# Performance work log

Hardware: AMD Instinct MI355X
Metric: run time of the kernel (lower is better)

Reference implementation:

```python
import jax, jax.numpy as jnp
import numpy as np

K = 1024      # num_embeddings
D = 256       # embedding_dim
BETA = 0.25
DECAY = 0.99
EPS = 1e-05


def setup_inputs() -> dict:
    key = jax.random.key(0)
    k1, k2 = jax.random.split(key)
    z_e = jax.random.normal(k1, (32, D, 32, 32), dtype=jnp.float32)
    embedding = jax.random.normal(k2, (K, D), dtype=jnp.float32)
    ema_cluster_size = jnp.zeros((K,), dtype=jnp.float32)
    ema_w = embedding  # buffer initialized as a clone of the codebook
    return {"z_e": z_e, "embedding": embedding,
            "ema_cluster_size": ema_cluster_size, "ema_w": ema_w}


def reference(z_e, embedding, ema_cluster_size, ema_w):
    B, Dd, H, W = z_e.shape
    # (B, D, H, W) -> (N, D)
    flat_z = jnp.transpose(z_e, (0, 2, 3, 1)).reshape(-1, Dd)

    # L2 distance argmin (||z||^2 + ||e||^2 - 2 z.e)
    dist = (jnp.sum(flat_z * flat_z, axis=1, keepdims=True)
            + jnp.sum(embedding * embedding, axis=1)
            - 2.0 * flat_z @ embedding.T)
    indices = jnp.argmin(dist, axis=1)  # (N,)

    # EMA update (operates on detached values; buffers updated in-place in torch)
    flat_z_sg = jax.lax.stop_gradient(flat_z)
    cluster_size = jax.ops.segment_sum(
        jnp.ones_like(indices, dtype=z_e.dtype), indices, num_segments=K)
    new_ema_cluster_size = DECAY * ema_cluster_size + (1.0 - DECAY) * cluster_size
    dw = jax.ops.segment_sum(flat_z_sg, indices, num_segments=K)  # one_hot.T @ flat_z
    new_ema_w = DECAY * ema_w + (1.0 - DECAY) * dw
    new_embedding = new_ema_w / (new_ema_cluster_size + EPS)[:, None]

    # Gather uses the *updated* codebook (torch copies into the buffer first)
    z_q_flat = new_embedding[indices]                      # (N, D)
    z_q = jnp.transpose(z_q_flat.reshape(B, H, W, Dd), (0, 3, 1, 2))

    # Straight-through estimator + commitment loss
    z_q_st = z_e + jax.lax.stop_gradient(z_q - z_e)
    vq_loss = BETA * jnp.mean((z_e - jax.lax.stop_gradient(z_q)) ** 2)

    return (z_q_st, vq_loss, indices.reshape(B, H, W),
            new_embedding, new_ema_cluster_size, new_ema_w)
```

## Files before the change

### kernel.cpp

```cpp
#include <hip/hip_runtime.h>
#include <stdint.h>

#define N_ROWS 32768
#define K_CODES 1024
#define D_DIM 256
#define NELEM 8388608

#define WS_COUNTS 0
#define WS_LOSS 1030
#define WS_ENORM 263168
#define WS_ROWBEST_BYTES 1056768
#define WS_IDX_BYTES 1318912

#define O_ZQ 0
#define O_LOSS 8388608
#define O_IDX 8388609
#define O_EMB 8421377
#define O_CS 8683521
#define O_EMAW 8684545

#define EP_BYTE_OFF 33685520

typedef _Float16 half8 __attribute__((ext_vector_type(8)));
typedef float f32x16 __attribute__((ext_vector_type(16)));

__device__ __forceinline__ unsigned int fenc(float f) {
    unsigned int u = __float_as_uint(f);
    return (u & 0x80000000u) ? ~u : (u | 0x80000000u);
}
__device__ __forceinline__ unsigned long long umin64(unsigned long long a, unsigned long long b) {
    return a < b ? a : b;
}
__device__ __forceinline__ void gll16(const void* g, void* l) {
    __builtin_amdgcn_global_load_lds((const __attribute__((address_space(1))) void*)g,
                                     (__attribute__((address_space(3))) void*)l, 16, 0, 0);
}

__global__ __launch_bounds__(256) void k_init(float* ws) {
    int i = blockIdx.x * 256 + threadIdx.x;
    if (i < 2048) ws[i] = 0.0f;
    unsigned long long* rb = (unsigned long long*)((char*)ws + WS_ROWBEST_BYTES);
    if (i < N_ROWS) rb[i] = 0xFFFFFFFFFFFFFFFFull;
}

__global__ __launch_bounds__(256) void k_conv_e(const float* __restrict__ emb,
                                                _Float16* __restrict__ Ep,
                                                float* __restrict__ enorm) {
    int k = blockIdx.x, d = threadIdx.x;
    float v = emb[k * 256 + d];
    _Float16 h = (_Float16)v;
    _Float16 l = (_Float16)(v - (float)h);
    int s = d >> 3, sub = d & 7;
    Ep[((size_t)s * 1024 + k) * 8 + sub] = h;
    Ep[((size_t)(32 + s) * 1024 + k) * 8 + sub] = l;
    float sq = v * v;
    #pragma unroll
    for (int off = 32; off >= 1; off >>= 1) sq += __shfl_down(sq, off, 64);
    __shared__ float red[4];
    if ((d & 63) == 0) red[d >> 6] = sq;
    __syncthreads();
    if (d == 0) enorm[k] = (red[0] + red[1]) + (red[2] + red[3]);
}

__global__ __launch_bounds__(256) void k_conv_z(const float* __restrict__ z_e,
                                                _Float16* __restrict__ Zp,
                                                float* __restrict__ lossacc) {
    __shared__ float lt[64 * 68];
    __shared__ float red[4];
    int t = threadIdx.x;
    int hw0 = blockIdx.x * 64, d0 = blockIdx.y * 64, b = blockIdx.z;
    const float* src = z_e + (size_t)b * 262144 + (size_t)d0 * 1024 + hw0;
    int dl = t >> 4, hl = (t & 15) * 4;
    float sq = 0.0f;
    #pragma unroll
    for (int i = 0; i < 4; i++) {
        int d = dl + i * 16;
        float4 v = *(const float4*)(src + (size_t)d * 1024 + hl);
        sq += v.x * v.x + v.y * v.y + v.z * v.z + v.w * v.w;
        lt[(hl + 0) * 68 + d] = v.x;
        lt[(hl + 1) * 68 + d] = v.y;
        lt[(hl + 2) * 68 + d] = v.z;
        lt[(hl + 3) * 68 + d] = v.w;
    }
    __syncthreads();
    int hr = t >> 2, seg = t & 3;
    int n = b * 1024 + hw0 + hr;
    int sg0 = (d0 >> 3) + seg * 2;
    half8 hi[2], lo[2];
    #pragma unroll
    for (int p = 0; p < 2; p++) {
        #pragma unroll
        for (int j = 0; j < 8; j++) {
            float v = lt[hr * 68 + seg * 16 + p * 8 + j];
            _Float16 h = (_Float16)v;
            hi[p][j] = h;
            lo[p][j] = (_Float16)(v - (float)h);
        }
    }
    *(half8*)(Zp + ((size_t)(sg0 + 0) * 32768 + n) * 8) = hi[0];
    *(half8*)(Zp + ((size_t)(sg0 + 1) * 32768 + n) * 8) = hi[1];
    *(half8*)(Zp + ((size_t)(32 + sg0) * 32768 + n) * 8) = lo[0];
    *(half8*)(Zp + ((size_t)(33 + sg0) * 32768 + n) * 8) = lo[1];
    #pragma unroll
    for (int off = 32; off >= 1; off >>= 1) sq += __shfl_down(sq, off, 64);
    if ((t & 63) == 0) red[t >> 6] = sq;
    __syncthreads();
    if (t == 0) atomicAdd(lossacc, (red[0] + red[1]) + (red[2] + red[3]));
}

__global__ __launch_bounds__(256) void k_mm(const _Float16* __restrict__ Zp,
                                            const _Float16* __restrict__ Ep,
                                            const float* __restrict__ enorm,
                                            unsigned long long* __restrict__ row_best) {
    __shared__ __align__(16) char smem[32768];
    _Float16* Za = (_Float16*)smem;
    _Float16* Ea = (_Float16*)(smem + 16384);
    unsigned long long* slot = (unsigned long long*)smem;

    int t = threadIdx.x;
    int lane = t & 63, wv = t >> 6;
    int b = blockIdx.x;
    int rt = (b & 7) + ((b >> 6) << 3);
    int ct = (b >> 3) & 7;
    int row0 = rt * 128, code0 = ct * 128;

    int wr = wv >> 1, wc = wv & 1;
    int m31 = lane & 31, ko = lane >> 5;

    f32x16 acc[2][2];
    #pragma unroll
    for (int i = 0; i < 2; i++)
        #pragma unroll
        for (int j = 0; j < 2; j++)
            #pragma unroll
            for (int r = 0; r < 16; r++) acc[i][j][r] = 0.0f;

    const char* zgl = (const char*)Zp + ((size_t)(2 * wv) * 32768 + row0 + lane) * 16;
    const char* egl = (const char*)Ep + ((size_t)(2 * wv) * 1024 + code0 + lane) * 16;
    _Float16* zld = Za + 2 * wv * 1024;
    _Float16* eld = Ea + 2 * wv * 1024;

    for (int c = 0; c < 12; c++) {
        int kz = (c < 8) ? c : (c - 8);
        int ge = (c < 4) ? c * 8 : (c < 8) ? (c - 4) * 8 : 32 + (c - 8) * 8;
        const char* zg = zgl + (size_t)kz * 8 * 32768 * 16;
        const char* eg = egl + (size_t)ge * 1024 * 16;
        gll16(zg, zld);
        gll16(zg + 64 * 16, zld + 512);
        gll16(zg + 32768 * 16, zld + 1024);
        gll16(zg + 32768 * 16 + 64 * 16, zld + 1536);
        gll16(eg, eld);
        gll16(eg + 64 * 16, eld + 512);
        gll16(eg + 1024 * 16, eld + 1024);
        gll16(eg + 1024 * 16 + 64 * 16, eld + 1536);
        __syncthreads();
        #pragma unroll
        for (int ks = 0; ks < 4; ks++) {
            int sseg = 2 * ks + ko;
            half8 a0 = *(const half8*)(Za + sseg * 1024 + (wr * 64 + m31) * 8);
            half8 a1 = *(const half8*)(Za + sseg * 1024 + (wr * 64 + 32 + m31) * 8);
            half8 b0 = *(const half8*)(Ea + sseg * 1024 + (wc * 64 + m31) * 8);
            half8 b1 = *(const half8*)(Ea + sseg * 1024 + (wc * 64 + 32 + m31) * 8);
            acc[0][0] = __builtin_amdgcn_mfma_f32_32x32x16_f16(a0, b0, acc[0][0], 0, 0, 0);
            acc[0][1] = __builtin_amdgcn_mfma_f32_32x32x16_f16(a0, b1, acc[0][1], 0, 0, 0);
            acc[1][0] = __builtin_amdgcn_mfma_f32_32x32x16_f16(a1, b0, acc[1][0], 0, 0, 0);
            acc[1][1] = __builtin_amdgcn_mfma_f32_32x32x16_f16(a1, b1, acc[1][1], 0, 0, 0);
        }
        __syncthreads();
    }

    float en0 = enorm[code0 + wc * 64 + m31];
    float en1 = enorm[code0 + wc * 64 + 32 + m31];
    unsigned int col0 = code0 + wc * 64 + m31;
    unsigned int col1 = col0 + 32;

    if (wc == 0) {
        #pragma unroll
        for (int mt = 0; mt < 2; mt++)
            #pragma unroll
            for (int j = 0; j < 16; j++) {
                int row = wr * 64 + mt * 32 + 4 * ko + (j & 3) + 8 * (j >> 2);
                unsigned long long p0 = ((unsigned long long)fenc(en0 - 2.0f * acc[mt][0][j]) << 32) | col0;
                unsigned long long p1 = ((unsigned long long)fenc(en1 - 2.0f * acc[mt][1][j]) << 32) | col1;
                slot[row * 32 + ((m31 + row) & 31)] = umin64(p0, p1);
            }
    }
    __syncthreads();
    if (wc == 1) {
        #pragma unroll
        for (int mt = 0; mt < 2; mt++)
            #pragma unroll
            for (int j = 0; j < 16; j++) {
                int row = wr * 64 + mt * 32 + 4 * ko + (j & 3) + 8 * (j >> 2);
                unsigned long long p0 = ((unsigned long long)fenc(en0 - 2.0f * acc[mt][0][j]) << 32) | col0;
                unsigned long long p1 = ((unsigned long long)fenc(en1 - 2.0f * acc[mt][1][j]) << 32) | col1;
                atomicMin(&slot[row * 32 + ((m31 + row) & 31)], umin64(p0, p1));
            }
    }
    __syncthreads();
    if (t < 128) {
        unsigned long long m = slot[t * 32 + (t & 31)];
        #pragma unroll
        for (int i = 1; i < 32; i++) m = umin64(m, slot[t * 32 + ((i + t) & 31)]);
        atomicMin(&row_best[row0 + t], m);
    }
}

__global__ __launch_bounds__(256) void k_fin_idx(const unsigned long long* __restrict__ rb,
                                                 int* __restrict__ idxs,
                                                 float* __restrict__ counts,
                                                 float* __restrict__ out) {
    __shared__ float hist[K_CODES];
    int t = threadIdx.x;
    #pragma unroll
    for (int j = 0; j < 4; j++) hist[j * 256 + t] = 0.0f;
    __syncthreads();
    int i = blockIdx.x * 256 + t;
    int id = (int)(rb[i] & 0xFFFFFFFFull);
    idxs[i] = id;
    out[O_IDX + i] = (float)id;
    atomicAdd(&hist[id], 1.0f);
    __syncthreads();
    #pragma unroll
    for (int j = 0; j < 4; j++) {
        float h = hist[j * 256 + t];
        if (h != 0.0f) atomicAdd(&counts[j * 256 + t], h);
    }
}

__global__ __launch_bounds__(256) void k_dw(const float* __restrict__ z_e,
                                            const int* __restrict__ idxs,
                                            float* __restrict__ part) {
    __shared__ float acc[K_CODES];
    int t = threadIdx.x;
    int s = blockIdx.x;
    int d = blockIdx.y;
    #pragma unroll
    for (int j = 0; j < 4; j++) acc[j * 256 + t] = 0.0f;
    __syncthreads();
    #pragma unroll
    for (int i = 0; i < 4; i++) {
        int b = s * 4 + i;
        int4 id4 = *(const int4*)(idxs + b * 1024 + t * 4);
        float4 v = *(const float4*)(z_e + (size_t)b * 262144 + (size_t)d * 1024 + t * 4);
        atomicAdd(&acc[id4.x], v.x);
        atomicAdd(&acc[id4.y], v.y);
        atomicAdd(&acc[id4.z], v.z);
        atomicAdd(&acc[id4.w], v.w);
    }
    __syncthreads();
    float* pr = part + ((size_t)s * 256 + d) * 1024;
    #pragma unroll
    for (int j = 0; j < 4; j++) pr[j * 256 + t] = acc[j * 256 + t];
}

__global__ __launch_bounds__(256) void k_red(const float* __restrict__ part,
                                             const float* __restrict__ ema_cs,
                                             const float* __restrict__ ema_w,
                                             const float* __restrict__ counts,
                                             float* __restrict__ lossacc,
                                             float* __restrict__ out) {
    __shared__ float tile[64 * 69];
    __shared__ float csl[64];
    __shared__ float craw[64];
    __shared__ float red[4];
    int t = threadIdx.x;
    int k0 = blockIdx.x * 64, d0 = blockIdx.y * 64;
    int dr = t >> 4, kc = t & 15;
    float4 sum[4] = {};
    for (int s = 0; s < 8; s++) {
        const float* pb = part + ((size_t)s * 256 + d0) * 1024 + k0 + kc * 4;
        #pragma unroll
        for (int q = 0; q < 4; q++) {
            float4 v = *(const float4*)(pb + (size_t)(dr + 16 * q) * 1024);
            sum[q].x += v.x; sum[q].y += v.y; sum[q].z += v.z; sum[q].w += v.w;
        }
    }
    if (t < 64) {
        float c = counts[k0 + t];
        craw[t] = c;
        csl[t] = 0.99f * ema_cs[k0 + t] + 0.01f * c;
    }
    #pragma unroll
    for (int q = 0; q < 4; q++) {
        float* p = tile + (dr + 16 * q) * 69 + kc * 4;
        p[0] = sum[q].x; p[1] = sum[q].y; p[2] = sum[q].z; p[3] = sum[q].w;
    }
    __syncthreads();
    int kk = t >> 2, dq = t & 3;
    int k = k0 + kk;
    float inv = 1.0f / (csl[kk] + 1e-5f);
    float cr = craw[kk];
    float lterm = 0.0f;
    #pragma unroll
    for (int j4 = 0; j4 < 4; j4++) {
        int dd = dq * 16 + j4 * 4;
        size_t kd = (size_t)k * 256 + d0 + dd;
        float4 w = *(const float4*)(ema_w + kd);
        float s0 = tile[(dd + 0) * 69 + kk];
        float s1 = tile[(dd + 1) * 69 + kk];
        float s2 = tile[(dd + 2) * 69 + kk];
        float s3 = tile[(dd + 3) * 69 + kk];
        float4 nw;
        nw.x = 0.99f * w.x + 0.01f * s0;
        nw.y = 0.99f * w.y + 0.01f * s1;
        nw.z = 0.99f * w.z + 0.01f * s2;
        nw.w = 0.99f * w.w + 0.01f * s3;
        *(float4*)(out + O_EMAW + kd) = nw;
        float4 ne = {nw.x * inv, nw.y * inv, nw.z * inv, nw.w * inv};
        *(float4*)(out + O_EMB + kd) = ne;
        lterm += ne.x * (cr * ne.x - 2.0f * s0);
        lterm += ne.y * (cr * ne.y - 2.0f * s1);
        lterm += ne.z * (cr * ne.z - 2.0f * s2);
        lterm += ne.w * (cr * ne.w - 2.0f * s3);
    }
    if (blockIdx.y == 0 && t < 64) out[O_CS + k0 + t] = csl[t];
    #pragma unroll
    for (int off = 32; off >= 1; off >>= 1) lterm += __shfl_down(lterm, off, 64);
    if ((t & 63) == 0) red[t >> 6] = lterm;
    __syncthreads();
    if (t == 0) atomicAdd(lossacc, (red[0] + red[1]) + (red[2] + red[3]));
}

__global__ __launch_bounds__(256) void k_bcast(const int* __restrict__ idxs,
                                               const float* __restrict__ lossacc,
                                               float* __restrict__ out) {
    __shared__ float lt[64 * 68];
    __shared__ int sid[64];
    int t = threadIdx.x;
    int hw0 = blockIdx.x * 64, d0 = blockIdx.y * 64, b = blockIdx.z;
    if (t < 64) sid[t] = idxs[b * 1024 + hw0 + t];
    __syncthreads();
    int r = t >> 2, c = t & 3;
    const float* nrow = out + O_EMB + (size_t)sid[r] * 256 + d0;
    #pragma unroll
    for (int it = 0; it < 4; it++) {
        int dd = it * 16 + c * 4;
        float4 q = *(const float4*)(nrow + dd);
        float* p = lt + r * 68 + dd;
        p[0] = q.x; p[1] = q.y; p[2] = q.z; p[3] = q.w;
    }
    __syncthreads();
    int dl = t >> 4, hl = (t & 15) * 4;
    float* dst = out + O_ZQ + (size_t)b * 262144 + (size_t)d0 * 1024 + hw0;
    #pragma unroll
    for (int i = 0; i < 4; i++) {
        int d = dl + i * 16;
        float4 w;
        w.x = lt[(hl + 0) * 68 + d];
        w.y = lt[(hl + 1) * 68 + d];
        w.z = lt[(hl + 2) * 68 + d];
        w.w = lt[(hl + 3) * 68 + d];
        *(float4*)(dst + (size_t)d * 1024 + hl) = w;
    }
    if (blockIdx.x == 0 && blockIdx.y == 0 && blockIdx.z == 0 && t == 0)
        out[O_LOSS] = lossacc[0] * 2.9802322387695312e-08f;
}

extern "C" void kernel_launch(void* const* d_in, const int* in_sizes, int n_in,
                              void* d_out, int out_size, void* d_ws, size_t ws_size,
                              hipStream_t stream) {
    const float* z_e = (const float*)d_in[0];
    const float* emb = (const float*)d_in[1];
    const float* ema_cs = (const float*)d_in[2];
    const float* ema_w = (const float*)d_in[3];
    float* out = (float*)d_out;
    float* ws = (float*)d_ws;

    float* counts = ws + WS_COUNTS;
    float* lossacc = ws + WS_LOSS;
    float* enorm = ws + WS_ENORM;
    unsigned long long* row_best = (unsigned long long*)((char*)d_ws + WS_ROWBEST_BYTES);
    int* idxs = (int*)((char*)d_ws + WS_IDX_BYTES);

    _Float16* Zp = (_Float16*)d_out;
    _Float16* Ep = (_Float16*)((char*)d_out + EP_BYTE_OFF);
    float* part = (float*)d_out;

    k_init<<<128, 256, 0, stream>>>(ws);
    k_conv_e<<<1024, 256, 0, stream>>>(emb, Ep, enorm);
    k_conv_z<<<dim3(16, 4, 32), 256, 0, stream>>>(z_e, Zp, lossacc);
    k_mm<<<2048, 256, 0, stream>>>(Zp, Ep, enorm, row_best);
    k_fin_idx<<<128, 256, 0, stream>>>(row_best, idxs, counts, out);
    k_dw<<<dim3(8, 256), 256, 0, stream>>>(z_e, idxs, part);
    k_red<<<dim3(16, 4), 256, 0, stream>>>(part, ema_cs, ema_w, counts, lossacc, out);
    k_bcast<<<dim3(16, 4, 32), 256, 0, stream>>>(idxs, lossacc, out);
}
```

Baseline: 240.5 us.

## Widen matmul code tile to 256 and rebuild dw scatter on fp16 packed rows

The distance matmul now computes 128x256 tiles per block instead of 128x128. Each wave holds 2x4 MFMA accumulators, and the loaded Z tile is reused across twice as many codes, with half as many blocks and a larger LDS buffer. The dw segment-sum kernel now reads the fp16 high half of the packed Z buffer, 8 dims per row, and scatters into a padded LDS histogram. Before, it read fp32 z_e one dim per block. This cuts global traffic and block count, but the dw sums lose the low-order fp16 bits, and the larger tile raises register and LDS pressure. The partial-sum buffer is also moved so it does not overlap the region dw now reads.

```diff
diff --git a/kernel.cpp b/kernel.cpp
--- a/kernel.cpp
+++ b/kernel.cpp
@@ -20,6 +20,7 @@
 #define O_EMAW 8684545
 
 #define EP_BYTE_OFF 33685520
+#define PART_BYTE_OFF 16777216
 
 typedef _Float16 half8 __attribute__((ext_vector_type(8)));
 typedef float f32x16 __attribute__((ext_vector_type(16)));
@@ -108,11 +109,11 @@
     if (t == 0) atomicAdd(lossacc, (red[0] + red[1]) + (red[2] + red[3]));
 }
 
-__global__ __launch_bounds__(256) void k_mm(const _Float16* __restrict__ Zp,
-                                            const _Float16* __restrict__ Ep,
-                                            const float* __restrict__ enorm,
-                                            unsigned long long* __restrict__ row_best) {
-    __shared__ __align__(16) char smem[32768];
+__global__ __launch_bounds__(256, 2) void k_mm(const _Float16* __restrict__ Zp,
+                                               const _Float16* __restrict__ Ep,
+                                               const float* __restrict__ enorm,
+                                               unsigned long long* __restrict__ row_best) {
+    __shared__ __align__(16) char smem[49152];
     _Float16* Za = (_Float16*)smem;
     _Float16* Ea = (_Float16*)(smem + 16384);
     unsigned long long* slot = (unsigned long long*)smem;
@@ -120,25 +121,25 @@
     int t = threadIdx.x;
     int lane = t & 63, wv = t >> 6;
     int b = blockIdx.x;
-    int rt = (b & 7) + ((b >> 6) << 3);
-    int ct = (b >> 3) & 7;
-    int row0 = rt * 128, code0 = ct * 128;
+    int rt = (b & 7) + ((b >> 5) << 3);
+    int ct = (b >> 3) & 3;
+    int row0 = rt * 128, code0 = ct * 256;
 
     int wr = wv >> 1, wc = wv & 1;
     int m31 = lane & 31, ko = lane >> 5;
 
-    f32x16 acc[2][2];
+    f32x16 acc[2][4];
     #pragma unroll
     for (int i = 0; i < 2; i++)
         #pragma unroll
-        for (int j = 0; j < 2; j++)
+        for (int j = 0; j < 4; j++)
             #pragma unroll
             for (int r = 0; r < 16; r++) acc[i][j][r] = 0.0f;
 
     const char* zgl = (const char*)Zp + ((size_t)(2 * wv) * 32768 + row0 + lane) * 16;
     const char* egl = (const char*)Ep + ((size_t)(2 * wv) * 1024 + code0 + lane) * 16;
     _Float16* zld = Za + 2 * wv * 1024;
-    _Float16* eld = Ea + 2 * wv * 1024;
+    _Float16* eld = Ea + 2 * wv * 2048;
 
     for (int c = 0; c < 12; c++) {
         int kz = (c < 8) ? c : (c - 8);
@@ -151,28 +152,41 @@
         gll16(zg + 32768 * 16 + 64 * 16, zld + 1536);
         gll16(eg, eld);
         gll16(eg + 64 * 16, eld + 512);
-        gll16(eg + 1024 * 16, eld + 1024);
-        gll16(eg + 1024 * 16 + 64 * 16, eld + 1536);
+        gll16(eg + 128 * 16, eld + 1024);
+        gll16(eg + 192 * 16, eld + 1536);
+        gll16(eg + 1024 * 16, eld + 2048);
+        gll16(eg + 1024 * 16 + 64 * 16, eld + 2560);
+        gll16(eg + 1024 * 16 + 128 * 16, eld + 3072);
+        gll16(eg + 1024 * 16 + 192 * 16, eld + 3584);
         __syncthreads();
         #pragma unroll
         for (int ks = 0; ks < 4; ks++) {
-            int sseg = 2 * ks + ko;
-            half8 a0 = *(const half8*)(Za + sseg * 1024 + (wr * 64 + m31) * 8);
-            half8 a1 = *(const half8*)(Za + sseg * 1024 + (wr * 64 + 32 + m31) * 8);
-            half8 b0 = *(const half8*)(Ea + sseg * 1024 + (wc * 64 + m31) * 8);
-            half8 b1 = *(const half8*)(Ea + sseg * 1024 + (wc * 64 + 32 + m31) * 8);
+            int ss = 2 * ks + ko;
+            half8 a0 = *(const half8*)(Za + ss * 1024 + (wr * 64 + m31) * 8);
+            half8 a1 = *(const half8*)(Za + ss * 1024 + (wr * 64 + 32 + m31) * 8);
+            half8 b0 = *(const half8*)(Ea + ss * 2048 + (wc * 128 + m31) * 8);
+            half8 b1 = *(const half8*)(Ea + ss * 2048 + (wc * 128 + 32 + m31) * 8);
+            half8 b2 = *(const half8*)(Ea + ss * 2048 + (wc * 128 + 64 + m31) * 8);
+            half8 b3 = *(const half8*)(Ea + ss * 2048 + (wc * 128 + 96 + m31) * 8);
             acc[0][0] = __builtin_amdgcn_mfma_f32_32x32x16_f16(a0, b0, acc[0][0], 0, 0, 0);
             acc[0][1] = __builtin_amdgcn_mfma_f32_32x32x16_f16(a0, b1, acc[0][1], 0, 0, 0);
+            acc[0][2] = __builtin_amdgcn_mfma_f32_32x32x16_f16(a0, b2, acc[0][2], 0, 0, 0);
+            acc[0][3] = __builtin_amdgcn_mfma_f32_32x32x16_f16(a0, b3, acc[0][3], 0, 0, 0);
             acc[1][0] = __builtin_amdgcn_mfma_f32_32x32x16_f16(a1, b0, acc[1][0], 0, 0, 0);
             acc[1][1] = __builtin_amdgcn_mfma_f32_32x32x16_f16(a1, b1, acc[1][1], 0, 0, 0);
+            acc[1][2] = __builtin_amdgcn_mfma_f32_32x32x16_f16(a1, b2, acc[1][2], 0, 0, 0);
+            acc[1][3] = __builtin_amdgcn_mfma_f32_32x32x16_f16(a1, b3, acc[1][3], 0, 0, 0);
         }
         __syncthreads();
     }
 
-    float en0 = enorm[code0 + wc * 64 + m31];
-    float en1 = enorm[code0 + wc * 64 + 32 + m31];
-    unsigned int col0 = code0 + wc * 64 + m31;
-    unsigned int col1 = col0 + 32;
+    float en_c[4];
+    unsigned int col_c[4];
+    #pragma unroll
+    for (int nt = 0; nt < 4; nt++) {
+        col_c[nt] = code0 + wc * 128 + nt * 32 + m31;
+        en_c[nt] = enorm[col_c[nt]];
+    }
 
     if (wc == 0) {
         #pragma unroll
@@ -180,9 +194,14 @@
             #pragma unroll
             for (int j = 0; j < 16; j++) {
                 int row = wr * 64 + mt * 32 + 4 * ko + (j & 3) + 8 * (j >> 2);
-                unsigned long long p0 = ((unsigned long long)fenc(en0 - 2.0f * acc[mt][0][j]) << 32) | col0;
-                unsigned long long p1 = ((unsigned long long)fenc(en1 - 2.0f * acc[mt][1][j]) << 32) | col1;
-                slot[row * 32 + ((m31 + row) & 31)] = umin64(p0, p1);
+                unsigned long long best = 0xFFFFFFFFFFFFFFFFull;
+                #pragma unroll
+                for (int nt = 0; nt < 4; nt++) {
+                    unsigned long long pk =
+                        ((unsigned long long)fenc(en_c[nt] - 2.0f * acc[mt][nt][j]) << 32) | col_c[nt];
+                    best = umin64(best, pk);
+                }
+                slot[row * 32 + ((m31 + row) & 31)] = best;
             }
     }
     __syncthreads();
@@ -192,9 +211,14 @@
             #pragma unroll
             for (int j = 0; j < 16; j++) {
                 int row = wr * 64 + mt * 32 + 4 * ko + (j & 3) + 8 * (j >> 2);
-                unsigned long long p0 = ((unsigned long long)fenc(en0 - 2.0f * acc[mt][0][j]) << 32) | col0;
-                unsigned long long p1 = ((unsigned long long)fenc(en1 - 2.0f * acc[mt][1][j]) << 32) | col1;
-                atomicMin(&slot[row * 32 + ((m31 + row) & 31)], umin64(p0, p1));
+                unsigned long long best = 0xFFFFFFFFFFFFFFFFull;
+                #pragma unroll
+                for (int nt = 0; nt < 4; nt++) {
+                    unsigned long long pk =
+                        ((unsigned long long)fenc(en_c[nt] - 2.0f * acc[mt][nt][j]) << 32) | col_c[nt];
+                    best = umin64(best, pk);
+                }
+                atomicMin(&slot[row * 32 + ((m31 + row) & 31)], best);
             }
     }
     __syncthreads();
@@ -228,30 +252,32 @@
     }
 }
 
-__global__ __launch_bounds__(256) void k_dw(const float* __restrict__ z_e,
+__global__ __launch_bounds__(256) void k_dw(const _Float16* __restrict__ Zp,
                                             const int* __restrict__ idxs,
                                             float* __restrict__ part) {
-    __shared__ float acc[K_CODES];
+    __shared__ float acc[K_CODES * 9];
     int t = threadIdx.x;
     int s = blockIdx.x;
-    int d = blockIdx.y;
-    #pragma unroll
-    for (int j = 0; j < 4; j++) acc[j * 256 + t] = 0.0f;
-    __syncthreads();
-    #pragma unroll
-    for (int i = 0; i < 4; i++) {
-        int b = s * 4 + i;
-        int4 id4 = *(const int4*)(idxs + b * 1024 + t * 4);
-        float4 v = *(const float4*)(z_e + (size_t)b * 262144 + (size_t)d * 1024 + t * 4);
-        atomicAdd(&acc[id4.x], v.x);
-        atomicAdd(&acc[id4.y], v.y);
-        atomicAdd(&acc[id4.z], v.z);
-        atomicAdd(&acc[id4.w], v.w);
-    }
-    __syncthreads();
-    float* pr = part + ((size_t)s * 256 + d) * 1024;
-    #pragma unroll
-    for (int j = 0; j < 4; j++) pr[j * 256 + t] = acc[j * 256 + t];
+    int g = blockIdx.y;
+    #pragma unroll
+    for (int j = 0; j < 36; j++) acc[j * 256 + t] = 0.0f;
+    __syncthreads();
+    #pragma unroll 4
+    for (int i = 0; i < 16; i++) {
+        int r = s * 4096 + i * 256 + t;
+        int id = idxs[r];
+        half8 z = *(const half8*)(Zp + ((size_t)g * 32768 + r) * 8);
+        #pragma unroll
+        for (int dd = 0; dd < 8; dd++)
+            atomicAdd(&acc[id * 9 + dd], (float)z[dd]);
+    }
+    __syncthreads();
+    #pragma unroll
+    for (int dd = 0; dd < 8; dd++) {
+        float* pr = part + ((size_t)s * 256 + g * 8 + dd) * 1024;
+        #pragma unroll
+        for (int j = 0; j < 4; j++) pr[j * 256 + t] = acc[(j * 256 + t) * 9 + dd];
+    }
 }
 
 __global__ __launch_bounds__(256) void k_red(const float* __restrict__ part,
@@ -375,14 +401,14 @@
 
     _Float16* Zp = (_Float16*)d_out;
     _Float16* Ep = (_Float16*)((char*)d_out + EP_BYTE_OFF);
-    float* part = (float*)d_out;
+    float* part = (float*)((char*)d_out + PART_BYTE_OFF);
 
     k_init<<<128, 256, 0, stream>>>(ws);
     k_conv_e<<<1024, 256, 0, stream>>>(emb, Ep, enorm);
     k_conv_z<<<dim3(16, 4, 32), 256, 0, stream>>>(z_e, Zp, lossacc);
-    k_mm<<<2048, 256, 0, stream>>>(Zp, Ep, enorm, row_best);
+    k_mm<<<1024, 256, 0, stream>>>(Zp, Ep, enorm, row_best);
     k_fin_idx<<<128, 256, 0, stream>>>(row_best, idxs, counts, out);
-    k_dw<<<dim3(8, 256), 256, 0, stream>>>(z_e, idxs, part);
+    k_dw<<<dim3(8, 32), 256, 0, stream>>>(Zp, idxs, part);
     k_red<<<dim3(16, 4), 256, 0, stream>>>(part, ema_cs, ema_w, counts, lossacc, out);
     k_bcast<<<dim3(16, 4, 32), 256, 0, stream>>>(idxs, lossacc, out);
 }
```

After: 246.5 us. 1.03x slower.
